# Kernel tuning notes

Measured on AMD Instinct MI355X. Metric: run time of the kernel, lower is better.

## Reference

```python
import jax, jax.numpy as jnp
import numpy as np

D, K, N, B, H, FF, L = 512, 32, 50000, 4096, 8, 2048, 6
EPS = 1e-5


def setup_inputs() -> dict:
    keys = iter(jax.random.split(jax.random.key(0), 16))

    def rn(shape, s=0.02):
        return jax.random.normal(next(keys), shape, dtype=jnp.float32) * s

    z = lambda shape: jnp.zeros(shape, jnp.float32)
    o = lambda shape: jnp.ones(shape, jnp.float32)
    cf = rn((N, D), 1.0)
    cf = cf / jnp.linalg.norm(cf, axis=-1, keepdims=True)  # buffer is pre-normalized in __init__
    return dict(
        x=rn((B, D), 1.0), concept_feats=cf,
        type_embedding=rn((2, D), 1.0), pos_embedding=rn((K, D), 1.0), class_embedding=rn((1, D), 1.0),
        sa_in_w=rn((L, 3 * D, D)), sa_in_b=z((L, 3 * D)), sa_out_w=rn((L, D, D)), sa_out_b=z((L, D)),
        ca_in_w=rn((L, 3 * D, D)), ca_in_b=z((L, 3 * D)), ca_out_w=rn((L, D, D)), ca_out_b=z((L, D)),
        lin1_w=rn((L, FF, D)), lin1_b=z((L, FF)), lin2_w=rn((L, D, FF)), lin2_b=z((L, D)),
        ln1_g=o((L, D)), ln1_b=z((L, D)), ln2_g=o((L, D)), ln2_b=z((L, D)), ln3_g=o((L, D)), ln3_b=z((L, D)),
        region_w=rn((D, D)), region_b=z((D,)),
    )


def _ln(t, g, b):
    m = jnp.mean(t, -1, keepdims=True)
    v = jnp.mean((t - m) ** 2, -1, keepdims=True)
    return (t - m) * jax.lax.rsqrt(v + EPS) * g + b


def _mha(q_in, kv_in, in_w, in_b, out_w, out_b):
    # torch nn.MultiheadAttention with packed in_proj (rows: q,k,v)
    d = q_in.shape[-1]
    hd = d // H
    wq, wk, wv = in_w[:d], in_w[d:2 * d], in_w[2 * d:]
    bq, bk, bv = in_b[:d], in_b[d:2 * d], in_b[2 * d:]
    q = (q_in @ wq.T + bq).reshape(q_in.shape[0], q_in.shape[1], H, hd)
    k = (kv_in @ wk.T + bk).reshape(kv_in.shape[0], kv_in.shape[1], H, hd)
    v = (kv_in @ wv.T + bv).reshape(kv_in.shape[0], kv_in.shape[1], H, hd)
    scale = 1.0 / float(np.sqrt(hd))
    a = jax.nn.softmax(jnp.einsum('bqhd,bkhd->bhqk', q, k) * scale, axis=-1)
    o = jnp.einsum('bhqk,bkhd->bqhd', a, v).reshape(q_in.shape)
    return o @ out_w.T + out_b


def _forward(x, concept_feats, type_embedding, pos_embedding, class_embedding,
             sa_in_w, sa_in_b, sa_out_w, sa_out_b, ca_in_w, ca_in_b, ca_out_w, ca_out_b,
             lin1_w, lin1_b, lin2_w, lin2_b, ln1_g, ln1_b, ln2_g, ln2_b, ln3_g, ln3_b,
             region_w, region_b):
    b = x.shape[0]
    score = x @ concept_feats.T                          # [B, N]
    s_r, idx = jax.lax.top_k(score, K)                   # [B, K]
    h_r = concept_feats[idx]                             # [B, K, D] gather
    w = jax.nn.softmax(s_r, axis=-1)
    kv_first = x[:, None, :] + type_embedding[0]         # [B, 1, D]
    kv_second = w[..., None] * h_r + pos_embedding + type_embedding[1]
    kv = jnp.concatenate([kv_first, kv_second], axis=1)  # [B, K+1, D]
    t = jnp.broadcast_to(class_embedding[None], (b, 1, D))  # cls token query
    for i in range(L):  # post-norm TransformerDecoder, dropout=0 (eval)
        t = _ln(t + _mha(t, t, sa_in_w[i], sa_in_b[i], sa_out_w[i], sa_out_b[i]), ln1_g[i], ln1_b[i])
        t = _ln(t + _mha(t, kv, ca_in_w[i], ca_in_b[i], ca_out_w[i], ca_out_b[i]), ln2_g[i], ln2_b[i])
        ff = jax.nn.relu(t @ lin1_w[i].T + lin1_b[i]) @ lin2_w[i].T + lin2_b[i]
        t = _ln(t + ff, ln3_g[i], ln3_b[i])
    fine = t[:, 0, :]
    fine = fine / jnp.linalg.norm(fine, axis=-1, keepdims=True)
    coarse = x @ region_w.T + region_b
    coarse = coarse / jnp.linalg.norm(coarse, axis=-1, keepdims=True)
    aug = coarse + fine
    return aug / jnp.linalg.norm(aug, axis=-1, keepdims=True)


def reference(x, concept_feats, type_embedding, pos_embedding, class_embedding,
              sa_in_w, sa_in_b, sa_out_w, sa_out_b, ca_in_w, ca_in_b, ca_out_w, ca_out_b,
              lin1_w, lin1_b, lin2_w, lin2_b, ln1_g, ln1_b, ln2_g, ln2_b, ln3_g, ln3_b,
              region_w, region_b):
    return _forward(x, concept_feats, type_embedding, pos_embedding, class_embedding,
                    sa_in_w, sa_in_b, sa_out_w, sa_out_b, ca_in_w, ca_in_b, ca_out_w, ca_out_b,
                    lin1_w, lin1_b, lin2_w, lin2_b, ln1_g, ln1_b, ln2_g, ln2_b, ln3_g, ln3_b,
                    region_w, region_b)
```

## Files before the change

kernel.cpp:

```cpp
#include <hip/hip_runtime.h>
#include <cstdint>

typedef unsigned short bfraw;
typedef __attribute__((ext_vector_type(8))) short short8;
typedef __attribute__((ext_vector_type(4))) float f32x4;
typedef __attribute__((ext_vector_type(4))) unsigned int u32x4;

#define DEV static __device__ __forceinline__

constexpr int NCHUNK = 8;
constexpr int CHUNK = 6250;
constexpr int CHUNK_LD = 6272;
constexpr int LAYERS = 6;

DEV float b2f(bfraw s) { return __uint_as_float(((unsigned)s) << 16); }
DEV bfraw f2b(float f) {
  unsigned u = __float_as_uint(f);
  u += 0x7FFFu + ((u >> 16) & 1u);
  return (bfraw)(u >> 16);
}
DEV float keyinv16(unsigned k) {
  unsigned raw = (k & 0x8000u) ? (k ^ 0x8000u) : (~k & 0xFFFFu);
  return b2f((bfraw)raw);
}

__global__ __launch_bounds__(256) void k_cvt(const float* __restrict__ src,
                                             bfraw* __restrict__ dst, int n4) {
  int i = blockIdx.x * 256 + threadIdx.x;
  if (i < n4) {
    float4 v = ((const float4*)src)[i];
    ushort4 o;
    o.x = f2b(v.x); o.y = f2b(v.y); o.z = f2b(v.z); o.w = f2b(v.w);
    ((ushort4*)dst)[i] = o;
  }
}

__global__ __launch_bounds__(256) void k_cvt_s(const float* __restrict__ src,
                                               bfraw* __restrict__ dst,
                                               int n4PerChunk, long srcStride4, int nch) {
  long i = (long)blockIdx.x * 256 + threadIdx.x;
  if (i < (long)n4PerChunk * nch) {
    int c = (int)(i / n4PerChunk);
    int j = (int)(i % n4PerChunk);
    float4 v = ((const float4*)src)[c * srcStride4 + j];
    ushort4 o;
    o.x = f2b(v.x); o.y = f2b(v.y); o.z = f2b(v.z); o.w = f2b(v.w);
    ((ushort4*)dst)[i] = o;
  }
}

__global__ __launch_bounds__(256) void k_tr(const float* __restrict__ sa_in_w,
                                            bfraw* __restrict__ WvT) {
  __shared__ float tile[32][33];
  const int tx = threadIdx.x & 31, ty = threadIdx.x >> 5;
  const int j0 = blockIdx.y * 32, k0 = blockIdx.x * 32;
  const long l = blockIdx.z;
#pragma unroll
  for (int p = 0; p < 4; ++p)
    tile[ty + p * 8][tx] = sa_in_w[(l * 1536 + 1024 + j0 + ty + p * 8) * 512 + k0 + tx];
  __syncthreads();
#pragma unroll
  for (int p = 0; p < 4; ++p)
    WvT[l * 262144 + (long)(k0 + ty + p * 8) * 512 + j0 + tx] = f2b(tile[tx][ty + p * 8]);
}

__global__ __launch_bounds__(256) void k_bsa(const float* __restrict__ sa_out_w,
                                             const float* __restrict__ sa_in_b,
                                             const float* __restrict__ sa_out_b,
                                             float* __restrict__ bsa) {
  __shared__ float bv[512];
  const int t = threadIdx.x;
  const long l = blockIdx.x;
  bv[t] = sa_in_b[l * 1536 + 1024 + t];
  bv[t + 256] = sa_in_b[l * 1536 + 1024 + t + 256];
  __syncthreads();
#pragma unroll
  for (int h = 0; h < 2; ++h) {
    int m = t + h * 256;
    const float* wr = sa_out_w + (l * 512 + m) * 512;
    float s = 0.f;
    for (int q = 0; q < 128; ++q) {
      float4 v = ((const float4*)wr)[q];
      s += v.x * bv[q * 4] + v.y * bv[q * 4 + 1] + v.z * bv[q * 4 + 2] + v.w * bv[q * 4 + 3];
    }
    bsa[l * 512 + m] = s + sa_out_b[l * 512 + m];
  }
}

template <int TM, bool OUTF32, bool OUTBF, bool RELU, bool BIAS, bool SWZ>
__global__ __launch_bounds__(256, 2) void k_gemm(
    const bfraw* __restrict__ A, int lda, long sA,
    const bfraw* __restrict__ B, int ldb, long sB,
    float* __restrict__ Cf, bfraw* __restrict__ Cb, int ldc, long sC,
    const float* __restrict__ bias, int sBias,
    int N, int K) {
  constexpr int WR = TM / 64;
  constexpr int CW = 32 * WR;
  constexpr int JT = CW / 16;
  constexpr int AP = TM / 32;
  constexpr int STAGE_B = TM * 64 * 2 + 128 * 64 * 2;
  constexpr int EPP = OUTF32 ? 132 : 136;
  constexpr int EP_B = OUTF32 ? TM * 132 * 4 : TM * 136 * 2;
  constexpr int SMEM_B = STAGE_B > EP_B ? STAGE_B : EP_B;
  __shared__ __align__(16) char smem[SMEM_B];
  bfraw* lsA = (bfraw*)smem;
  bfraw* lsB = (bfraw*)(smem + TM * 64 * 2);
  const int t = threadIdx.x;
  const int lane = t & 63;
  const int wave = t >> 6;
  const int wr = (TM == 128) ? (wave & 1) : 0;
  const int wc = (TM == 128) ? (wave >> 1) : wave;
  int bx, by;
  if (SWZ) {
    int l = blockIdx.x;
    int xcd = l & 7;
    int s = l >> 3;
    by = s / 7;
    int bxi = s % 7;
    bx = bxi * 8 + xcd;
    if (bx * 128 >= N) return;
  } else {
    bx = blockIdx.x;
    by = blockIdx.y;
  }
  const int z = blockIdx.z;
  A += (long)z * sA;
  B += (long)z * sB;

  const int sRow = t >> 3;
  const int sCh = t & 7;
  const int rowA0 = by * TM;
  const int colB0 = bx * 128;

  f32x4 acc[4][JT];
#pragma unroll
  for (int i = 0; i < 4; ++i)
#pragma unroll
    for (int j = 0; j < JT; ++j) {
      acc[i][j][0] = 0.f; acc[i][j][1] = 0.f; acc[i][j][2] = 0.f; acc[i][j][3] = 0.f;
    }

  const int nk = K >> 6;
  const bfraw* aSrc[AP];
#pragma unroll
  for (int p = 0; p < AP; ++p) {
    int fr = p * 32 + sRow;
    int kc = sCh ^ (fr & 7);
    aSrc[p] = A + (long)(rowA0 + fr) * lda + kc * 8;
  }
  const bfraw* bSrc[4];
#pragma unroll
  for (int p = 0; p < 4; ++p) {
    int fr = p * 32 + sRow;
    int kc = sCh ^ (fr & 7);
    int rB = colB0 + fr;
    if (rB >= N) rB = N - 1;
    bSrc[p] = B + (long)rB * ldb + kc * 8;
  }

  for (int kt = 0; kt < nk; ++kt) {
    __syncthreads();
#pragma unroll
    for (int p = 0; p < AP; ++p)
      __builtin_amdgcn_global_load_lds(
          (const unsigned int*)(aSrc[p] + kt * 64),
          (unsigned int*)(smem + p * 4096 + wave * 1024), 16, 0, 0);
#pragma unroll
    for (int p = 0; p < 4; ++p)
      __builtin_amdgcn_global_load_lds(
          (const unsigned int*)(bSrc[p] + kt * 64),
          (unsigned int*)(smem + TM * 128 + p * 4096 + wave * 1024), 16, 0, 0);
    __syncthreads();
#pragma unroll
    for (int ks = 0; ks < 2; ++ks) {
      short8 af[4], bfm[JT];
#pragma unroll
      for (int i = 0; i < 4; ++i) {
        int r = wr * 64 + i * 16 + (lane & 15);
        int q = ks * 4 + (lane >> 4);
        af[i] = *(const short8*)(lsA + r * 64 + ((q ^ (r & 7)) * 8));
      }
#pragma unroll
      for (int j = 0; j < JT; ++j) {
        int n = wc * CW + j * 16 + (lane & 15);
        int q = ks * 4 + (lane >> 4);
        bfm[j] = *(const short8*)(lsB + n * 64 + ((q ^ (n & 7)) * 8));
      }
#pragma unroll
      for (int i = 0; i < 4; ++i)
#pragma unroll
        for (int j = 0; j < JT; ++j)
          acc[i][j] = __builtin_amdgcn_mfma_f32_16x16x32_bf16(af[i], bfm[j], acc[i][j], 0, 0, 0);
    }
  }

  __syncthreads();
  const int Nrem = N - colB0;
  if (OUTBF) {
    unsigned short* ep = (unsigned short*)smem;
#pragma unroll
    for (int j = 0; j < JT; ++j) {
      int cl = wc * CW + j * 16 + (lane & 15);
      int n = colB0 + cl;
      float bv = 0.f;
      if (BIAS) bv = (n < N) ? bias[(long)z * sBias + n] : 0.f;
#pragma unroll
      for (int i = 0; i < 4; ++i) {
        int r0 = wr * 64 + i * 16 + ((lane >> 4) << 2);
#pragma unroll
        for (int r = 0; r < 4; ++r) {
          float v = acc[i][j][r] + bv;
          if (RELU) v = fmaxf(v, 0.f);
          ep[(r0 + r) * EPP + cl] = f2b(v);
        }
      }
    }
    __syncthreads();
#pragma unroll
    for (int pass = 0; pass < TM / 16; ++pass) {
      int row = pass * 16 + (t >> 4);
      int c0 = (t & 15) * 8;
      long base = (long)(rowA0 + row) * ldc + (long)z * sC + colB0;
      if (c0 + 8 <= Nrem) {
        u32x4 v = *(const u32x4*)(ep + row * EPP + c0);
        *(u32x4*)(Cb + base + c0) = v;
      } else if (c0 < Nrem) {
        for (int q = c0; q < Nrem && q < 128; ++q) Cb[base + q] = (bfraw)ep[row * EPP + q];
      }
    }
  }
  if (OUTF32) {
    float* ep = (float*)smem;
#pragma unroll
    for (int j = 0; j < JT; ++j) {
      int cl = wc * CW + j * 16 + (lane & 15);
      int n = colB0 + cl;
      float bv = 0.f;
      if (BIAS) bv = (n < N) ? bias[(long)z * sBias + n] : 0.f;
#pragma unroll
      for (int i = 0; i < 4; ++i) {
        int r0 = wr * 64 + i * 16 + ((lane >> 4) << 2);
#pragma unroll
        for (int r = 0; r < 4; ++r) {
          float v = acc[i][j][r] + bv;
          if (RELU) v = fmaxf(v, 0.f);
          ep[(r0 + r) * EPP + cl] = v;
        }
      }
    }
    __syncthreads();
#pragma unroll
    for (int pass = 0; pass < TM / 8; ++pass) {
      int row = pass * 8 + (t >> 5);
      int c0 = (t & 31) * 4;
      long base = (long)(rowA0 + row) * ldc + (long)z * sC + colB0;
      if (c0 + 4 <= Nrem) {
        f32x4 v = *(const f32x4*)(ep + row * EPP + c0);
        *(f32x4*)(Cf + base + c0) = v;
      } else if (c0 < Nrem) {
        for (int q = c0; q < Nrem && q < 128; ++q) Cf[base + q] = ep[row * EPP + q];
      }
    }
  }
}

__global__ __launch_bounds__(256) void k_select(const bfraw* __restrict__ scores,
                                                float* __restrict__ cval, int* __restrict__ cidx,
                                                int chunk) {
  __shared__ unsigned short keys[CHUNK];
  __shared__ unsigned hist[256];
  __shared__ unsigned sh_sel, sh_rank, cnt_a, cnt_t;
  __shared__ unsigned tiebuf[64];
  const int t = threadIdx.x;
  const long b = blockIdx.x;
  const bfraw* row = scores + b * CHUNK_LD;
  for (int i = t; i < CHUNK; i += 256) {
    unsigned u = row[i];
    keys[i] = (u & 0x8000u) ? (unsigned short)(~u) : (unsigned short)(u | 0x8000u);
  }
  if (t == 0) { cnt_a = 0; cnt_t = 0; }
  unsigned prefix = 0, pmask = 0, rank = 64;
  for (int lev = 0; lev < 2; ++lev) {
    const int sh = 8 - lev * 8;
    hist[t] = 0;
    __syncthreads();
    for (int i = t; i < CHUNK; i += 256) {
      unsigned k = keys[i];
      if ((k & pmask) == prefix) atomicAdd(&hist[(k >> sh) & 255u], 1u);
    }
    __syncthreads();
    if (t < 64) {
      unsigned h0 = hist[t * 4], h1 = hist[t * 4 + 1], h2 = hist[t * 4 + 2], h3 = hist[t * 4 + 3];
      unsigned lsum = h0 + h1 + h2 + h3;
      unsigned suf = lsum;
#pragma unroll
      for (int off = 1; off < 64; off <<= 1) {
        unsigned vv = __shfl_down(suf, off);
        if (t + off < 64) suf += vv;
      }
      unsigned c = suf - lsum;
      unsigned hs[4] = {h0, h1, h2, h3};
#pragma unroll
      for (int q = 3; q >= 0; --q) {
        if (rank > c && rank <= c + hs[q]) { sh_sel = (unsigned)(t * 4 + q); sh_rank = rank - c; }
        c += hs[q];
      }
    }
    __syncthreads();
    prefix |= sh_sel << sh;
    pmask |= 255u << sh;
    rank = sh_rank;
    __syncthreads();
  }
  const unsigned cutkey = prefix;
  float* ov = cval + (b * NCHUNK + chunk) * 64;
  int* oi = cidx + (b * NCHUNK + chunk) * 64;
  for (int i = t; i < CHUNK; i += 256) {
    unsigned k = keys[i];
    if (k > cutkey) {
      unsigned p = atomicAdd(&cnt_a, 1u);
      ov[p] = keyinv16(k);
      oi[p] = chunk * CHUNK + i;
    } else if (k == cutkey) {
      unsigned p = atomicAdd(&cnt_t, 1u);
      if (p < 64) tiebuf[p] = (unsigned)i;
    }
  }
  __syncthreads();
  if (t == 0) {
    int need = (int)rank;
    int tc = cnt_t < 64u ? (int)cnt_t : 64;
    int base = (int)cnt_a;
    float cv = keyinv16(cutkey);
    for (int s2 = 0; s2 < need; ++s2) {
      unsigned best = 0xFFFFFFFFu; int bq = 0;
      for (int q2 = 0; q2 < tc; ++q2)
        if (tiebuf[q2] < best) { best = tiebuf[q2]; bq = q2; }
      tiebuf[bq] = 0xFFFFFFFFu;
      ov[base + s2] = cv;
      oi[base + s2] = chunk * CHUNK + (int)best;
    }
  }
}

__global__ __launch_bounds__(256) void k_refine(const float* __restrict__ cval,
                                                const int* __restrict__ cidx,
                                                const float* __restrict__ x,
                                                const float* __restrict__ cf,
                                                int* __restrict__ tidx, float* __restrict__ w) {
  __shared__ float sv[512];
  __shared__ int si[512];
  __shared__ float xs[512];
  __shared__ float rv[64];
  __shared__ int ri[64];
  const int t = threadIdx.x;
  const int lane = t & 63, wave = t >> 6;
  const long b = blockIdx.x;
  sv[t] = cval[b * 512 + t]; sv[t + 256] = cval[b * 512 + t + 256];
  si[t] = cidx[b * 512 + t]; si[t + 256] = cidx[b * 512 + t + 256];
  xs[t] = x[b * 512 + t]; xs[t + 256] = x[b * 512 + t + 256];
  __syncthreads();
  for (int k = 2; k <= 512; k <<= 1)
    for (int j = k >> 1; j >= 1; j >>= 1) {
      int i = ((t & ~(j - 1)) << 1) | (t & (j - 1));
      int p = i | j;
      bool dir = ((i & k) == 0);
      float va = sv[i], vb = sv[p];
      int ia = si[i], ib = si[p];
      bool pBetter = (vb > va) || (vb == va && ib < ia);
      if (pBetter == dir) { sv[i] = vb; sv[p] = va; si[i] = ib; si[p] = ia; }
      __syncthreads();
    }
  float xr[8];
  {
    float4 a = *(const float4*)(xs + lane * 8);
    float4 b2 = *(const float4*)(xs + lane * 8 + 4);
    xr[0] = a.x; xr[1] = a.y; xr[2] = a.z; xr[3] = a.w;
    xr[4] = b2.x; xr[5] = b2.y; xr[6] = b2.z; xr[7] = b2.w;
  }
#pragma unroll
  for (int k = 0; k < 16; ++k) {
    int c = wave * 16 + k;
    int idx = si[c];
    const float* cr = cf + (long)idx * 512 + lane * 8;
    float4 v0 = *(const float4*)cr;
    float4 v1 = *(const float4*)(cr + 4);
    float s = v0.x * xr[0] + v0.y * xr[1] + v0.z * xr[2] + v0.w * xr[3]
            + v1.x * xr[4] + v1.y * xr[5] + v1.z * xr[6] + v1.w * xr[7];
#pragma unroll
    for (int off = 1; off < 64; off <<= 1) s += __shfl_xor(s, off);
    if (lane == 0) { rv[c] = s; ri[c] = idx; }
  }
  __syncthreads();
  if (t < 64) {
    float v = rv[t];
    int ix = ri[t];
    for (int k = 2; k <= 64; k <<= 1)
      for (int j = k >> 1; j >= 1; j >>= 1) {
        float ov = __shfl_xor(v, j);
        int oi = __shfl_xor(ix, j);
        bool up = ((t & k) == 0);
        bool low = ((t & j) == 0);
        bool oBetter = (ov > v) || (ov == v && oi < ix);
        if (oBetter == (up == low)) { v = ov; ix = oi; }
      }
    float m = __shfl(v, 0);
    float e = (t < 32) ? __expf(v - m) : 0.f;
    float ssum = e;
#pragma unroll
    for (int off = 1; off < 64; off <<= 1) ssum += __shfl_xor(ssum, off);
    if (t < 32) {
      w[b * 32 + t] = e / ssum;
      tidx[b * 32 + t] = ix;
    }
  }
}

__global__ __launch_bounds__(256) void k_buildkv(const float* __restrict__ x, const bfraw* __restrict__ cfb,
                                                 const float* __restrict__ type_emb,
                                                 const float* __restrict__ pos_emb,
                                                 const float* __restrict__ w, const int* __restrict__ tidx,
                                                 bfraw* __restrict__ kv) {
  const int t = threadIdx.x;
  const long b = blockIdx.x;
  bfraw* out = kv + b * (33 * 512);
  const float* xr = x + b * 512;
  for (int d = t; d < 512; d += 256) out[d] = f2b(xr[d] + type_emb[d]);
  for (int j = 0; j < 32; ++j) {
    const long ci = tidx[b * 32 + j];
    const float wj = w[b * 32 + j];
    const bfraw* cr = cfb + ci * 512;
    bfraw* o = out + (j + 1) * 512;
    for (int d = t; d < 512; d += 256)
      o[d] = f2b(wj * b2f(cr[d]) + pos_emb[j * 512 + d] + type_emb[512 + d]);
  }
}

__global__ __launch_bounds__(256) void k_init_t(const float* __restrict__ cls, float* __restrict__ tf,
                                                bfraw* __restrict__ tb) {
  const long i = (long)blockIdx.x * 256 + threadIdx.x;
  const int d = (int)(i & 511);
  tf[i] = cls[d];
  tb[i] = f2b(cls[d]);
}

__global__ __launch_bounds__(256) void k_prep(const float* __restrict__ ca_in_w, bfraw* __restrict__ wkT) {
  const long o = (long)blockIdx.x * 256 + threadIdx.x;
  const int e = (int)(o & 63);
  long r = o >> 6;
  const int d = (int)(r & 511); r >>= 9;
  const int h = (int)(r & 7);
  const int i = (int)(r >> 3);
  wkT[o] = f2b(ca_in_w[((long)i * 1536 + 512 + h * 64 + e) * 512 + d]);
}

__global__ __launch_bounds__(256) void k_attn(const bfraw* __restrict__ u, const bfraw* __restrict__ kv,
                                              bfraw* __restrict__ cout) {
  __shared__ __align__(16) bfraw kvs[33 * 512];
  __shared__ __align__(16) bfraw us[8 * 512];
  __shared__ float ps[8 * 48];
  const int t = threadIdx.x, lane = t & 63, wave = t >> 6;
  const long b = blockIdx.x;
  const bfraw* kvg = kv + b * (33 * 512);
  const bfraw* ug = u + b * (8 * 512);

  {
#pragma unroll
    for (int r = 0; r < 8; ++r) {
      int row = r * 4 + wave;
      int sc = (lane & 56) | ((lane & 7) ^ (row & 7));
      __builtin_amdgcn_global_load_lds((const unsigned int*)(kvg + row * 512 + sc * 8),
                                       (unsigned int*)(kvs + row * 512), 16, 0, 0);
    }
    if (wave == 0)
      __builtin_amdgcn_global_load_lds((const unsigned int*)(kvg + 32 * 512 + lane * 8),
                                       (unsigned int*)(kvs + 32 * 512), 16, 0, 0);
#pragma unroll
    for (int r = 0; r < 2; ++r) {
      int row = r * 4 + wave;
      int sc = (lane & 56) | ((lane & 7) ^ (row & 7));
      __builtin_amdgcn_global_load_lds((const unsigned int*)(ug + row * 512 + sc * 8),
                                       (unsigned int*)(us + row * 512), 16, 0, 0);
    }
  }
  __syncthreads();

  if (wave < 2) {
    const int jj = wave * 16 + (lane & 15);
    const int rr = lane & 7;
    f32x4 acc = {0.f, 0.f, 0.f, 0.f};
#pragma unroll
    for (int ks = 0; ks < 16; ++ks) {
      int q = ks * 4 + (lane >> 4);
      short8 af = *(const short8*)(us + rr * 512 + (((q & 56) | ((q & 7) ^ rr)) * 8));
      short8 bf = *(const short8*)(kvs + jj * 512 + (((q & 56) | ((q & 7) ^ (jj & 7))) * 8));
      acc = __builtin_amdgcn_mfma_f32_16x16x32_bf16(af, bf, acc, 0, 0, 0);
    }
#pragma unroll
    for (int r = 0; r < 4; ++r) {
      int row = (lane >> 4) * 4 + r;
      if (row < 8) ps[row * 48 + wave * 16 + (lane & 15)] = acc[r] * 0.125f;
    }
  } else if (wave == 2) {
    int h = lane >> 3, seg = lane & 7;
    float s = 0.f;
#pragma unroll
    for (int i = 0; i < 8; ++i) {
      int c = seg * 8 + i;
      short8 kk = *(const short8*)(kvs + 32 * 512 + c * 8);
      short8 uu = *(const short8*)(us + h * 512 + (((c & 56) | ((c & 7) ^ h)) * 8));
#pragma unroll
      for (int e = 0; e < 8; ++e) s += b2f((bfraw)uu[e]) * b2f((bfraw)kk[e]);
    }
    s += __shfl_xor(s, 1);
    s += __shfl_xor(s, 2);
    s += __shfl_xor(s, 4);
    if (seg == 0) ps[h * 48 + 32] = s * 0.125f;
  }
  __syncthreads();

#pragma unroll
  for (int hh = 0; hh < 2; ++hh) {
    int h = wave + hh * 4;
    float sv2 = (lane < 33) ? ps[h * 48 + lane] : -3.0e38f;
    float m = sv2;
#pragma unroll
    for (int off = 1; off < 64; off <<= 1) m = fmaxf(m, __shfl_xor(m, off));
    float e = (lane < 33) ? __expf(sv2 - m) : 0.f;
    float s = e;
#pragma unroll
    for (int off = 1; off < 64; off <<= 1) s += __shfl_xor(s, off);
    if (lane < 33) ps[h * 48 + lane] = e / s;
  }
  __syncthreads();

#pragma unroll
  for (int hh = 0; hh < 2; ++hh) {
    int h = wave + hh * 4;
    float acc[8] = {0.f, 0.f, 0.f, 0.f, 0.f, 0.f, 0.f, 0.f};
    for (int j = 0; j < 33; ++j) {
      float pj = ps[h * 48 + j];
      int c = (lane & 56) | ((lane & 7) ^ (j & 7));
      short8 kk = *(const short8*)(kvs + j * 512 + c * 8);
#pragma unroll
      for (int q = 0; q < 8; ++q) acc[q] += pj * b2f((bfraw)kk[q]);
    }
    union { bfraw o[8]; uint4 v4; } pk;
#pragma unroll
    for (int q = 0; q < 8; ++q) pk.o[q] = f2b(acc[q]);
    *(uint4*)(cout + (b * 8 + h) * 512 + lane * 8) = pk.v4;
  }
}

__global__ __launch_bounds__(256) void k_ln(float* __restrict__ tf, bfraw* __restrict__ tb,
                                            const float* __restrict__ delta,
                                            const float* __restrict__ g, const float* __restrict__ be) {
  const int lane = threadIdx.x & 63, wave = threadIdx.x >> 6;
  const long row = (long)blockIdx.x * 4 + wave;
  float* tr = tf + row * 512;
  const float* dr = delta + row * 512;
  float v[8];
  float4 a0 = *(const float4*)(tr + lane * 8);
  float4 a1 = *(const float4*)(tr + lane * 8 + 4);
  float4 d0 = *(const float4*)(dr + lane * 8);
  float4 d1 = *(const float4*)(dr + lane * 8 + 4);
  v[0] = a0.x + d0.x; v[1] = a0.y + d0.y; v[2] = a0.z + d0.z; v[3] = a0.w + d0.w;
  v[4] = a1.x + d1.x; v[5] = a1.y + d1.y; v[6] = a1.z + d1.z; v[7] = a1.w + d1.w;
  float s = 0.f;
#pragma unroll
  for (int q = 0; q < 8; ++q) s += v[q];
#pragma unroll
  for (int off = 1; off < 64; off <<= 1) s += __shfl_xor(s, off);
  const float mean = s * (1.f / 512.f);
  float sq = 0.f;
#pragma unroll
  for (int q = 0; q < 8; ++q) { float d = v[q] - mean; sq += d * d; }
#pragma unroll
  for (int off = 1; off < 64; off <<= 1) sq += __shfl_xor(sq, off);
  const float rs = 1.f / sqrtf(sq * (1.f / 512.f) + 1e-5f);
  float4 g0 = *(const float4*)(g + lane * 8);
  float4 g1 = *(const float4*)(g + lane * 8 + 4);
  float4 b0 = *(const float4*)(be + lane * 8);
  float4 b1 = *(const float4*)(be + lane * 8 + 4);
  float gg[8] = {g0.x, g0.y, g0.z, g0.w, g1.x, g1.y, g1.z, g1.w};
  float bb[8] = {b0.x, b0.y, b0.z, b0.w, b1.x, b1.y, b1.z, b1.w};
  float o[8];
  union { bfraw u16[8]; uint4 u4; } pk;
#pragma unroll
  for (int q = 0; q < 8; ++q) {
    o[q] = (v[q] - mean) * rs * gg[q] + bb[q];
    pk.u16[q] = f2b(o[q]);
  }
  *(float4*)(tr + lane * 8) = make_float4(o[0], o[1], o[2], o[3]);
  *(float4*)(tr + lane * 8 + 4) = make_float4(o[4], o[5], o[6], o[7]);
  *(uint4*)(tb + row * 512 + lane * 8) = pk.u4;
}

__global__ __launch_bounds__(64) void k_final(const float* __restrict__ tf, const float* __restrict__ coarse,
                                              float* __restrict__ out) {
  const int lane = threadIdx.x;
  const long b = blockIdx.x;
  const float* fr = tf + b * 512;
  const float* cr = coarse + b * 512;
  float4 f0 = *(const float4*)(fr + lane * 8);
  float4 f1 = *(const float4*)(fr + lane * 8 + 4);
  float4 c0 = *(const float4*)(cr + lane * 8);
  float4 c1 = *(const float4*)(cr + lane * 8 + 4);
  float f[8] = {f0.x, f0.y, f0.z, f0.w, f1.x, f1.y, f1.z, f1.w};
  float c[8] = {c0.x, c0.y, c0.z, c0.w, c1.x, c1.y, c1.z, c1.w};
  float sf = 0.f, sc = 0.f;
#pragma unroll
  for (int q = 0; q < 8; ++q) { sf += f[q] * f[q]; sc += c[q] * c[q]; }
#pragma unroll
  for (int off = 1; off < 64; off <<= 1) { sf += __shfl_xor(sf, off); sc += __shfl_xor(sc, off); }
  const float rf = 1.f / sqrtf(sf), rc = 1.f / sqrtf(sc);
  float a[8];
  float sa = 0.f;
#pragma unroll
  for (int q = 0; q < 8; ++q) { a[q] = f[q] * rf + c[q] * rc; sa += a[q] * a[q]; }
#pragma unroll
  for (int off = 1; off < 64; off <<= 1) sa += __shfl_xor(sa, off);
  const float ra = 1.f / sqrtf(sa);
  *(float4*)(out + b * 512 + lane * 8) = make_float4(a[0] * ra, a[1] * ra, a[2] * ra, a[3] * ra);
  *(float4*)(out + b * 512 + lane * 8 + 4) = make_float4(a[4] * ra, a[5] * ra, a[6] * ra, a[7] * ra);
}

constexpr long OFF_XB = 0;
constexpr long OFF_WKT = 4194304;
constexpr long OFF_SAOUT = 7340032;
constexpr long OFF_WSAB = 10485760;
constexpr long OFF_CAWQ = 13631488;
constexpr long OFF_CAWV = 16777216;
constexpr long OFF_CAOUT = 19922944;
constexpr long OFF_REGW = 23068672;
constexpr long OFF_L1B = 23592960;
constexpr long OFF_L2B = 36175872;
constexpr long OFF_BSA = 48758784;
constexpr long OFF_TIDX = 48775168;
constexpr long OFF_WSM = 49299456;
constexpr long OFF_REGION = 49823744;
constexpr long OFF_POOL = 188235776;
constexpr long P_TF = 0;
constexpr long P_TB = 8388608;
constexpr long P_QBF = 12582912;
constexpr long P_UBUF = 16777216;
constexpr long P_CBUF = 50331648;
constexpr long WS_TOTAL = OFF_POOL + 83886080;

extern "C" void kernel_launch(void* const* d_in, const int* in_sizes, int n_in,
                              void* d_out, int out_size, void* d_ws, size_t ws_size,
                              hipStream_t stream) {
  if (n_in < 25) return;
  if (ws_size < (size_t)WS_TOTAL) return;

  const float* x = (const float*)d_in[0];
  const float* cf = (const float*)d_in[1];
  const float* type_emb = (const float*)d_in[2];
  const float* pos_emb = (const float*)d_in[3];
  const float* cls = (const float*)d_in[4];
  const float* sa_in_w = (const float*)d_in[5];
  const float* sa_in_b = (const float*)d_in[6];
  const float* sa_out_w = (const float*)d_in[7];
  const float* sa_out_b = (const float*)d_in[8];
  const float* ca_in_w = (const float*)d_in[9];
  const float* ca_in_b = (const float*)d_in[10];
  const float* ca_out_w = (const float*)d_in[11];
  const float* ca_out_b = (const float*)d_in[12];
  const float* lin1_w = (const float*)d_in[13];
  const float* lin1_b = (const float*)d_in[14];
  const float* lin2_w = (const float*)d_in[15];
  const float* lin2_b = (const float*)d_in[16];
  const float* ln1_g = (const float*)d_in[17];
  const float* ln1_bp = (const float*)d_in[18];
  const float* ln2_g = (const float*)d_in[19];
  const float* ln2_bp = (const float*)d_in[20];
  const float* ln3_g = (const float*)d_in[21];
  const float* ln3_bp = (const float*)d_in[22];
  const float* region_w = (const float*)d_in[23];
  const float* region_b = (const float*)d_in[24];

  char* ws = (char*)d_ws;
  bfraw* xb = (bfraw*)(ws + OFF_XB);
  bfraw* wkT = (bfraw*)(ws + OFF_WKT);
  bfraw* saout = (bfraw*)(ws + OFF_SAOUT);
  bfraw* wsab = (bfraw*)(ws + OFF_WSAB);
  bfraw* cawq = (bfraw*)(ws + OFF_CAWQ);
  bfraw* cawv = (bfraw*)(ws + OFF_CAWV);
  bfraw* caout = (bfraw*)(ws + OFF_CAOUT);
  bfraw* regw = (bfraw*)(ws + OFF_REGW);
  bfraw* l1b = (bfraw*)(ws + OFF_L1B);
  bfraw* l2b = (bfraw*)(ws + OFF_L2B);
  float* bsa = (float*)(ws + OFF_BSA);
  int* tidx = (int*)(ws + OFF_TIDX);
  float* wsm = (float*)(ws + OFF_WSM);
  bfraw* WvT = (bfraw*)(ws + OFF_REGION);
  bfraw* scoreb = (bfraw*)(ws + OFF_REGION);
  bfraw* kv = (bfraw*)(ws + OFF_REGION);
  char* pool = ws + OFF_POOL;
  float* tf = (float*)(pool + P_TF);
  float* cval = (float*)(pool + P_TF);
  bfraw* tb = (bfraw*)(pool + P_TB);
  int* cidx = (int*)(pool + P_TB);
  bfraw* qbf = (bfraw*)(pool + P_QBF);
  bfraw* tmpb = (bfraw*)(pool + P_QBF);
  bfraw* ubuf = (bfraw*)(pool + P_UBUF);
  bfraw* ffb = (bfraw*)(pool + P_UBUF);
  bfraw* cfb = (bfraw*)(pool + P_UBUF);
  bfraw* cbuf = (bfraw*)(pool + P_CBUF);
  float* delta = (float*)(pool + P_CBUF);
  float* coarse = (float*)(pool + P_CBUF + 8388608);

  dim3 blk(256);

  k_cvt<<<2048, blk, 0, stream>>>(x, xb, 524288);
  k_cvt<<<25000, blk, 0, stream>>>(cf, cfb, 6400000);
  k_cvt<<<1536, blk, 0, stream>>>(sa_out_w, saout, 393216);
  k_cvt<<<1536, blk, 0, stream>>>(ca_out_w, caout, 393216);
  k_cvt<<<256, blk, 0, stream>>>(region_w, regw, 65536);
  k_cvt<<<6144, blk, 0, stream>>>(lin1_w, l1b, 1572864);
  k_cvt<<<6144, blk, 0, stream>>>(lin2_w, l2b, 1572864);
  k_cvt_s<<<1536, blk, 0, stream>>>(ca_in_w, cawq, 65536, 196608, 6);
  k_cvt_s<<<1536, blk, 0, stream>>>(ca_in_w + 1024 * 512, cawv, 65536, 196608, 6);
  k_prep<<<6144, blk, 0, stream>>>(ca_in_w, wkT);
  k_tr<<<dim3(16, 16, 6), blk, 0, stream>>>(sa_in_w, WvT);
  k_gemm<64, false, true, false, false, false><<<dim3(4, 8, 6), blk, 0, stream>>>(
      saout, 512, 262144, WvT, 512, 262144, nullptr, wsab, 512, 262144, nullptr, 0, 512, 512);
  k_bsa<<<6, blk, 0, stream>>>(sa_out_w, sa_in_b, sa_out_b, bsa);

  for (int c = 0; c < NCHUNK; ++c) {
    k_gemm<128, false, true, false, false, true><<<dim3(1792, 1, 1), blk, 0, stream>>>(
        xb, 512, 0, cfb + (long)c * CHUNK * 512, 512, 0,
        nullptr, scoreb, CHUNK_LD, 0, nullptr, 0, CHUNK, 512);
    k_select<<<4096, blk, 0, stream>>>(scoreb, cval, cidx, c);
  }
  k_refine<<<4096, blk, 0, stream>>>(cval, cidx, x, cf, tidx, wsm);
  k_buildkv<<<4096, blk, 0, stream>>>(x, cfb, type_emb, pos_emb, wsm, tidx, kv);
  k_init_t<<<8192, blk, 0, stream>>>(cls, tf, tb);

  for (int i = 0; i < LAYERS; ++i) {
    const bfraw* ca_wq = cawq + (long)i * 262144;
    const float* ca_bq = ca_in_b + (long)i * 1536;
    const bfraw* ca_wv = cawv + (long)i * 262144;
    const float* ca_bv = ca_in_b + (long)i * 1536 + 1024;
    const bfraw* ca_wo = caout + (long)i * 262144;
    const float* ca_bo = ca_out_b + (long)i * 512;
    const bfraw* wkTi = wkT + (long)i * 8 * 512 * 64;

    k_gemm<64, true, false, false, true, false><<<dim3(4, 64, 1), blk, 0, stream>>>(
        tb, 512, 0, wsab + (long)i * 262144, 512, 0, delta, nullptr, 512, 0, bsa + i * 512, 0, 512, 512);
    k_ln<<<1024, blk, 0, stream>>>(tf, tb, delta, ln1_g + i * 512, ln1_bp + i * 512);

    k_gemm<64, false, true, false, true, false><<<dim3(4, 64, 1), blk, 0, stream>>>(
        tb, 512, 0, ca_wq, 512, 0, nullptr, qbf, 512, 0, ca_bq, 0, 512, 512);
    k_gemm<64, false, true, false, false, false><<<dim3(4, 64, 8), blk, 0, stream>>>(
        qbf, 512, 64, wkTi, 64, 32768, nullptr, ubuf, 4096, 512, nullptr, 0, 512, 64);
    k_attn<<<4096, blk, 0, stream>>>(ubuf, kv, cbuf);
    k_gemm<64, false, true, false, true, false><<<dim3(1, 64, 8), blk, 0, stream>>>(
        cbuf, 4096, 512, ca_wv, 512, 32768, nullptr, tmpb, 512, 64, ca_bv, 64, 64, 512);
    k_gemm<64, true, false, false, true, false><<<dim3(4, 64, 1), blk, 0, stream>>>(
        tmpb, 512, 0, ca_wo, 512, 0, delta, nullptr, 512, 0, ca_bo, 0, 512, 512);
    k_ln<<<1024, blk, 0, stream>>>(tf, tb, delta, ln2_g + i * 512, ln2_bp + i * 512);

    k_gemm<64, false, true, true, true, false><<<dim3(16, 64, 1), blk, 0, stream>>>(
        tb, 512, 0, l1b + (long)i * 1048576, 512, 0, nullptr, ffb, 2048, 0, lin1_b + i * 2048, 0, 2048, 512);
    k_gemm<64, true, false, false, true, false><<<dim3(4, 64, 1), blk, 0, stream>>>(
        ffb, 2048, 0, l2b + (long)i * 1048576, 2048, 0, delta, nullptr, 512, 0, lin2_b + i * 512, 0, 512, 2048);
    k_ln<<<1024, blk, 0, stream>>>(tf, tb, delta, ln3_g + i * 512, ln3_bp + i * 512);
  }

  k_gemm<64, true, false, false, true, false><<<dim3(4, 64, 1), blk, 0, stream>>>(
      xb, 512, 0, regw, 512, 0, coarse, nullptr, 512, 0, region_b, 0, 512, 512);
  k_final<<<4096, dim3(64), 0, stream>>>(tf, coarse, (float*)d_out);
}
```

Baseline: 2.423 ms.

## Double-buffer GEMM LDS tiles with async prefetch two stages ahead

Turns the GEMM main loop from a single-buffer load→sync→compute scheme into a two-buffer pipeline. Tile kt+2 is issued with global_load_lds into the freed buffer while tile kt is computed, and partial vmcnt waits let loads overlap MFMA work. This doubles the staging LDS footprint, which may reduce occupancy at launch_bounds(256,2). It also depends on hand-counted vmcnt values matching the number of loads issued per stage.

```diff
diff --git a/kernel.cpp b/kernel.cpp
--- a/kernel.cpp
+++ b/kernel.cpp
@@ -98,13 +98,13 @@
   constexpr int CW = 32 * WR;
   constexpr int JT = CW / 16;
   constexpr int AP = TM / 32;
-  constexpr int STAGE_B = TM * 64 * 2 + 128 * 64 * 2;
+  constexpr int ABYT = TM * 128;
+  constexpr int TILEB = ABYT + 128 * 128;
+  constexpr int STAGE_B = 2 * TILEB;
   constexpr int EPP = OUTF32 ? 132 : 136;
   constexpr int EP_B = OUTF32 ? TM * 132 * 4 : TM * 136 * 2;
   constexpr int SMEM_B = STAGE_B > EP_B ? STAGE_B : EP_B;
   __shared__ __align__(16) char smem[SMEM_B];
-  bfraw* lsA = (bfraw*)smem;
-  bfraw* lsB = (bfraw*)(smem + TM * 64 * 2);
   const int t = threadIdx.x;
   const int lane = t & 63;
   const int wave = t >> 6;
@@ -158,19 +158,33 @@
     bSrc[p] = B + (long)rB * ldb + kc * 8;
   }
 
-  for (int kt = 0; kt < nk; ++kt) {
-    __syncthreads();
+  auto stage = [&](int kt, int buf) {
 #pragma unroll
     for (int p = 0; p < AP; ++p)
       __builtin_amdgcn_global_load_lds(
           (const unsigned int*)(aSrc[p] + kt * 64),
-          (unsigned int*)(smem + p * 4096 + wave * 1024), 16, 0, 0);
+          (unsigned int*)(smem + buf * TILEB + p * 4096 + wave * 1024), 16, 0, 0);
 #pragma unroll
     for (int p = 0; p < 4; ++p)
       __builtin_amdgcn_global_load_lds(
           (const unsigned int*)(bSrc[p] + kt * 64),
-          (unsigned int*)(smem + TM * 128 + p * 4096 + wave * 1024), 16, 0, 0);
-    __syncthreads();
+          (unsigned int*)(smem + buf * TILEB + ABYT + p * 4096 + wave * 1024), 16, 0, 0);
+  };
+
+  stage(0, 0);
+  if (nk > 1) stage(1, 1);
+  int cur = 0;
+  for (int kt = 0; kt < nk; ++kt) {
+    if (kt + 1 < nk) {
+      if constexpr (TM == 128) asm volatile("s_waitcnt vmcnt(8)" ::: "memory");
+      else asm volatile("s_waitcnt vmcnt(6)" ::: "memory");
+    } else {
+      asm volatile("s_waitcnt vmcnt(0)" ::: "memory");
+    }
+    __builtin_amdgcn_s_barrier();
+    __builtin_amdgcn_sched_barrier(0);
+    const bfraw* lsA = (const bfraw*)(smem + cur * TILEB);
+    const bfraw* lsB = (const bfraw*)(smem + cur * TILEB + ABYT);
 #pragma unroll
     for (int ks = 0; ks < 2; ++ks) {
       short8 af[4], bfm[JT];
@@ -192,6 +206,9 @@
         for (int j = 0; j < JT; ++j)
           acc[i][j] = __builtin_amdgcn_mfma_f32_16x16x32_bf16(af[i], bfm[j], acc[i][j], 0, 0, 0);
     }
+    __builtin_amdgcn_s_barrier();
+    if (kt + 2 < nk) stage(kt + 2, cur);
+    cur ^= 1;
   }
 
   __syncthreads();
```

Result: faster. 2.226 ms (-8.2%).
